# Kernel tuning notes

Measured on AMD Instinct MI355X. Metric: run time of the kernel, lower is better.

The kernel has to match this reference:

```python
import jax, jax.numpy as jnp
import numpy as np

B, S, D, H = 2, 2048, 1024, 16
HD = D // H  # 64


def setup_inputs() -> dict:
    key = jax.random.key(0)
    ks = jax.random.split(key, 6)
    x = jax.random.normal(ks[0], (B, S, D), dtype=jnp.float32)
    # rotary frequencies: theta = 10000^{-2i/hd}, angles = pos * theta
    inv_freq = 1.0 / (10000.0 ** (jnp.arange(0, HD, 2, dtype=jnp.float32) / HD))  # [HD/2]
    angles = jnp.arange(S, dtype=jnp.float32)[:, None] * inv_freq[None, :]  # [S, HD/2]
    freqs_cos = jnp.cos(angles)
    freqs_sin = jnp.sin(angles)
    scale = 0.02
    w_qkv = jax.random.normal(ks[1], (3 * D, D), dtype=jnp.float32) * scale
    b_qkv = jnp.zeros((3 * D,), dtype=jnp.float32)
    w_dense = jax.random.normal(ks[2], (D, D), dtype=jnp.float32) * scale
    b_dense = jnp.zeros((D,), dtype=jnp.float32)
    return {"x": x, "w_qkv": w_qkv, "b_qkv": b_qkv, "w_dense": w_dense,
            "b_dense": b_dense, "freqs_cos": freqs_cos, "freqs_sin": freqs_sin}


def _apply_rope(t, cos, sin):
    # t: [B, S, H, HD]; cos/sin: [S, HD/2] broadcast as [1, S, 1, HD/2]
    tr = t.reshape(t.shape[:-1] + (HD // 2, 2))
    x0, x1 = tr[..., 0], tr[..., 1]
    c = cos[None, :, None, :]
    s = sin[None, :, None, :]
    o0 = x0 * c - x1 * s  # real part of complex multiply
    o1 = x0 * s + x1 * c  # imag part
    return jnp.stack([o0, o1], axis=-1).reshape(t.shape)


def reference(x, w_qkv, b_qkv, w_dense, b_dense, freqs_cos, freqs_sin):
    b, s, d = x.shape
    qkv = x @ w_qkv.T + b_qkv              # [B, S, 3D]
    qkv = qkv.reshape(b, s, 3, H, HD)
    q, k, v = qkv[:, :, 0], qkv[:, :, 1], qkv[:, :, 2]  # [B, S, H, HD]
    q = _apply_rope(q, freqs_cos, freqs_sin)
    k = _apply_rope(k, freqs_cos, freqs_sin)
    # causal SDPA, scale = 1/sqrt(head_dim)
    q = q.transpose(0, 2, 1, 3)  # [B, H, S, HD]
    k = k.transpose(0, 2, 1, 3)
    v = v.transpose(0, 2, 1, 3)
    scores = jnp.einsum('bhqd,bhkd->bhqk', q, k) / jnp.sqrt(jnp.float32(HD))
    causal = jnp.tril(jnp.ones((s, s), dtype=bool))
    scores = jnp.where(causal[None, None], scores, jnp.finfo(scores.dtype).min)
    attn = jax.nn.softmax(scores, axis=-1)
    ctx = jnp.einsum('bhqk,bhkd->bhqd', attn, v)   # [B, H, S, HD]
    ctx = ctx.transpose(0, 2, 1, 3).reshape(b, s, d)
    return ctx @ w_dense.T + b_dense
```

## Files before the change

kernel.cpp:

```cpp
#include <hip/hip_runtime.h>
#include <stdint.h>

#define Bb 2
#define Ss 2048
#define Dd 1024
#define Hh 16
#define HDd 64

typedef float f32x4 __attribute__((ext_vector_type(4)));
typedef __bf16 bf16x8 __attribute__((ext_vector_type(8)));
typedef __bf16 bf16x2 __attribute__((ext_vector_type(2)));
typedef short s16x8 __attribute__((ext_vector_type(8)));

__device__ inline unsigned short f2bf(float f) {
  unsigned u = __builtin_bit_cast(unsigned, f);
  u += 0x7fffu + ((u >> 16) & 1u);
  return (unsigned short)(u >> 16);
}
__device__ inline float bf2f(unsigned short h) {
  unsigned u = ((unsigned)h) << 16;
  return __builtin_bit_cast(float, u);
}
__device__ inline unsigned pkcvt(float a, float b) {
  bf16x2 v;
  v[0] = (__bf16)a;
  v[1] = (__bf16)b;
  return __builtin_bit_cast(unsigned, v);
}
__device__ inline float ex2(float x) {
#if __has_builtin(__builtin_amdgcn_exp2f)
  return __builtin_amdgcn_exp2f(x);
#else
  float r;
  asm("v_exp_f32 %0, %1\n\ts_nop 1" : "=v"(r) : "v"(x));
  return r;
#endif
}
__device__ inline int swz(int row, int soff) {
  return (row << 6) + ((((soff >> 3) ^ (row & 7)) << 3) | (soff & 7));
}

#define GLDS(dst, src)                                                        \
  __builtin_amdgcn_global_load_lds(                                           \
      (const __attribute__((address_space(1))) void*)(src),                   \
      (__attribute__((address_space(3))) void*)(dst), 16, 0, 0)

__global__ void cast_all(const float* __restrict__ x, const float* __restrict__ wq,
                         const float* __restrict__ wd, unsigned short* __restrict__ dst) {
  int i = blockIdx.x * blockDim.x + threadIdx.x;
  float4 v;
  if (i < 1048576) v = ((const float4*)x)[i];
  else if (i < 1835008) v = ((const float4*)wq)[i - 1048576];
  else v = ((const float4*)wd)[i - 1835008];
  ushort4 o;
  o.x = f2bf(v.x); o.y = f2bf(v.y); o.z = f2bf(v.z); o.w = f2bf(v.w);
  ((ushort4*)dst)[i] = o;
}

__global__ __launch_bounds__(512, 2) void gemm_qkv(
    const unsigned short* __restrict__ A, const unsigned short* __restrict__ Bw,
    const float* __restrict__ bias, unsigned short* __restrict__ qkvout,
    unsigned short* __restrict__ vtout,
    const float* __restrict__ fc, const float* __restrict__ fs) {
  const int K = 1024, NT = 16;
  __shared__ __align__(16) unsigned short Ah[2][2][128 * 32];
  __shared__ __align__(16) unsigned short Bh[2][2][192 * 32];
  const int tid = threadIdx.x;
  const int w = tid >> 6, l = tid & 63;
  const int lg = l >> 4, lr = l & 15;
  const int wm = w >> 2, wn = w & 3;
  int id = blockIdx.y * gridDim.x + blockIdx.x;
  const int nwg = gridDim.x * gridDim.y;
  id = (id & 7) * (nwg >> 3) + (id >> 3);
  const int bx = id % gridDim.x, by = id / gridDim.x;
  const int mbase = by * 128, nbase = bx * 192;

  const unsigned short *as0, *bs0, *bs1, *bs2;
  {
    int r_ = tid >> 2, s_ = (tid & 3) ^ ((r_ >> 1) & 3);
    as0 = A + (size_t)(mbase + r_) * K + s_ * 8;
    bs0 = Bw + (size_t)(nbase + r_) * K + s_ * 8;
    int cb2 = 512 + tid;
    int h2 = cb2 >= 768;
    int cw2 = cb2 - h2 * 768;
    int r2 = cw2 >> 2, s2 = (cw2 & 3) ^ ((r2 >> 1) & 3);
    bs1 = Bw + (size_t)(nbase + r2) * K + h2 * 32 + s2 * 8;
    int cw3 = 256 + tid;
    int r3 = cw3 >> 2, s3 = (cw3 & 3) ^ ((r3 >> 1) & 3);
    bs2 = Bw + (size_t)(nbase + r3) * K + 32 + s3 * 8;
  }
#define STAGE(buf, k0)                                                        \
  GLDS(&Ah[buf][0][0] + tid * 8, as0 + (k0));                                 \
  GLDS(&Ah[buf][0][0] + 4096 + tid * 8, as0 + 32 + (k0));                     \
  GLDS(&Bh[buf][0][0] + tid * 8, bs0 + (k0));                                 \
  GLDS(&Bh[buf][0][0] + (512 + tid) * 8, bs1 + (k0));                         \
  GLDS(&Bh[buf][0][0] + (1024 + tid) * 8, bs2 + (k0));

  STAGE(0, 0);
  __syncthreads();

  f32x4 acc[4][3] = {};
  for (int t = 0; t < NT; ++t) {
    const int cur = t & 1;
    if (t + 1 < NT) { STAGE(cur ^ 1, (t + 1) * 64); }
#pragma unroll
    for (int h = 0; h < 2; ++h) {
      bf16x8 bfr[3], af[4];
#pragma unroll
      for (int ni = 0; ni < 3; ++ni) {
        int row = wn * 48 + ni * 16 + lr;
        bfr[ni] = *(const bf16x8*)(&Bh[cur][h][row * 32 + ((lg ^ ((row >> 1) & 3)) << 3)]);
      }
#pragma unroll
      for (int j = 0; j < 4; ++j) {
        int row = wm * 64 + j * 16 + lr;
        af[j] = *(const bf16x8*)(&Ah[cur][h][row * 32 + ((lg ^ ((row >> 1) & 3)) << 3)]);
      }
      __builtin_amdgcn_s_setprio(1);
#pragma unroll
      for (int j = 0; j < 4; ++j)
#pragma unroll
        for (int ni = 0; ni < 3; ++ni)
          acc[j][ni] = __builtin_amdgcn_mfma_f32_16x16x32_bf16(
              af[j], bfr[ni], acc[j][ni], 0, 0, 0);
      __builtin_amdgcn_s_setprio(0);
    }
    __syncthreads();
  }
#undef STAGE

#pragma unroll
  for (int mi = 0; mi < 4; ++mi)
#pragma unroll
    for (int ni = 0; ni < 3; ++ni) {
      int col = nbase + wn * 48 + ni * 16 + lr;
      float bi = bias[col];
      int row0 = mbase + wm * 64 + mi * 16 + lg * 4;
      float o4[4];
#pragma unroll
      for (int r = 0; r < 4; ++r) o4[r] = acc[mi][ni][r] + bi;
      int sect = col >> 10;
      int d = col & 63;
      int srow0 = row0 & 2047;
      if (sect < 2) {
        int p = d >> 1;
#pragma unroll
        for (int r = 0; r < 4; ++r) {
          float vp = __shfl_xor(o4[r], 1);
          float c = fc[(srow0 + r) * 32 + p];
          float s = fs[(srow0 + r) * 32 + p];
          float o = (d & 1) ? (vp * s + o4[r] * c) : (o4[r] * c - vp * s);
          qkvout[(size_t)(row0 + r) * 3072 + col] = f2bf(o);
        }
      } else {
        int bh = (row0 >> 11) * 16 + ((col >> 6) & 15);
        uint2 o;
        o.x = pkcvt(o4[0], o4[1]);
        o.y = pkcvt(o4[2], o4[3]);
        *(uint2*)&vtout[((size_t)(bh * 64 + d)) * 2048 + srow0] = o;
      }
    }
}

__global__ __launch_bounds__(256) void gemm_bt(
    const unsigned short* __restrict__ A, const unsigned short* __restrict__ Bw,
    const float* __restrict__ bias, float* __restrict__ Cout,
    int M, int N, int K) {
  __shared__ __align__(16) unsigned short As[128 * 32];
  __shared__ __align__(16) unsigned short Bs[128 * 32];
  const int tid = threadIdx.x;
  const int w = tid >> 6, l = tid & 63;
  const int lg = l >> 4, lr = l & 15;
  const int mbase = blockIdx.y * 128, nbase = blockIdx.x * 128;
  const int wr = w >> 1, wc = w & 1;
  f32x4 acc[4][4] = {};

  for (int k0 = 0; k0 < K; k0 += 32) {
#pragma unroll
    for (int r = 0; r < 2; ++r) {
      int c = r * 256 + w * 64 + l;
      int row = c >> 2, c8 = c & 3;
      GLDS(As + c * 8, A + (size_t)(mbase + row) * K + k0 + c8 * 8);
      GLDS(Bs + c * 8, Bw + (size_t)(nbase + row) * K + k0 + c8 * 8);
    }
    __syncthreads();
    bf16x8 af[4], bfr[4];
#pragma unroll
    for (int mi = 0; mi < 4; ++mi)
      af[mi] = *(const bf16x8*)(As + (wr * 64 + mi * 16 + lr) * 32 + lg * 8);
#pragma unroll
    for (int ni = 0; ni < 4; ++ni)
      bfr[ni] = *(const bf16x8*)(Bs + (wc * 64 + ni * 16 + lr) * 32 + lg * 8);
#pragma unroll
    for (int mi = 0; mi < 4; ++mi)
#pragma unroll
      for (int ni = 0; ni < 4; ++ni)
        acc[mi][ni] = __builtin_amdgcn_mfma_f32_16x16x32_bf16(
            af[mi], bfr[ni], acc[mi][ni], 0, 0, 0);
    __syncthreads();
  }

#pragma unroll
  for (int mi = 0; mi < 4; ++mi) {
#pragma unroll
    for (int ni = 0; ni < 4; ++ni) {
      int col = nbase + wc * 64 + ni * 16 + lr;
      float bi = bias[col];
#pragma unroll
      for (int r = 0; r < 4; ++r) {
        int row = mbase + wr * 64 + mi * 16 + lg * 4 + r;
        Cout[(size_t)row * N + col] = acc[mi][ni][r] + bi;
      }
    }
  }
}

__global__ __launch_bounds__(256, 3) void attn(
    const unsigned short* __restrict__ qkv, const unsigned short* __restrict__ vt,
    unsigned short* __restrict__ ctx) {
  __shared__ __align__(16) unsigned short Ks[2][64 * 64];
  __shared__ __align__(16) unsigned short Vs[2][64 * 64];
  __shared__ __align__(16) unsigned short Ps[4][32 * 64];
  int did = blockIdx.x;
  int x = did & 7, rest = did >> 3;
  int bh = x * 4 + (rest & 3);
  int qi = 31 - (rest >> 2);
  int b = bh >> 4, h = bh & 15;
  int qbase = qi * 64;
  int tid = threadIdx.x;
  int w = tid >> 6, l = tid & 63;
  int lg = l >> 4, lr = l & 15;
  int wq = w & 1, wk = w >> 1;
  int qw = wq * 32;

  bf16x8 qb[2][2];
#pragma unroll
  for (int mi = 0; mi < 2; ++mi)
#pragma unroll
    for (int kc = 0; kc < 2; ++kc) {
      s16x8 qr = *(const s16x8*)(qkv +
          (size_t)(b * Ss + qbase + qw + mi * 16 + lr) * 3072 + h * 64 + kc * 32 + lg * 8);
      bf16x8 qs;
#pragma unroll
      for (int e = 0; e < 8; ++e)
        qs[e] = (__bf16)(bf2f((unsigned short)qr[e]) * 0.18033688f);
      qb[mi][kc] = qs;
    }

  int c1 = tid, c2 = 256 + tid;
  int r1 = c1 >> 3, s1 = ((c1 & 7) ^ (r1 & 7)) * 8;
  int r2 = c2 >> 3, s2 = ((c2 & 7) ^ (r2 & 7)) * 8;
  const unsigned short* kg1 = qkv + ((size_t)(b * Ss) + r1) * 3072 + 1024 + h * 64 + s1;
  const unsigned short* kg2 = qkv + ((size_t)(b * Ss) + r2) * 3072 + 1024 + h * 64 + s2;
  const unsigned short* vg1 = vt + ((size_t)bh * 64 + r1) * 2048 + s1;
  const unsigned short* vg2 = vt + ((size_t)bh * 64 + r2) * 2048 + s2;
#define STAGEKV(kt)                                                           \
  {                                                                           \
    int tt_ = (kt) & 1;                                                       \
    GLDS(&Ks[tt_][0] + c1 * 8, kg1 + (size_t)(kt) * 64 * 3072);               \
    GLDS(&Ks[tt_][0] + c2 * 8, kg2 + (size_t)(kt) * 64 * 3072);               \
    GLDS(&Vs[tt_][0] + c1 * 8, vg1 + (kt) * 64);                              \
    GLDS(&Vs[tt_][0] + c2 * 8, vg2 + (kt) * 64);                              \
  }

  int nkt = qi + 1;
  int nsup = (nkt + 1) >> 1;

  STAGEKV(0);
  if (1 < nkt) STAGEKV(1);
  __syncthreads();

  f32x4 acc[4][2] = {};
  float mrow[2] = {-1e30f, -1e30f}, lsum[2] = {0.f, 0.f};

  for (int j = 0; j < nsup; ++j) {
    int kt = 2 * j + wk;
    if (kt < nkt) {
      f32x4 st[4][2] = {};
      __builtin_amdgcn_s_setprio(1);
#pragma unroll
      for (int kc = 0; kc < 2; ++kc) {
#pragma unroll
        for (int ni = 0; ni < 4; ++ni) {
          bf16x8 ka = *(const bf16x8*)&Ks[wk][swz(ni * 16 + lr, kc * 32 + lg * 8)];
#pragma unroll
          for (int mi = 0; mi < 2; ++mi)
            st[ni][mi] = __builtin_amdgcn_mfma_f32_16x16x32_bf16(
                ka, qb[mi][kc], st[ni][mi], 0, 0, 0);
        }
      }
      __builtin_amdgcn_s_setprio(0);

      float tm[2] = {-1e30f, -1e30f};
      if (kt == qi) {
#pragma unroll
        for (int mi = 0; mi < 2; ++mi) {
          int rq = qw + mi * 16 + lr;
#pragma unroll
          for (int ni = 0; ni < 4; ++ni)
#pragma unroll
            for (int r4 = 0; r4 < 4; ++r4) {
              float s = st[ni][mi][r4];
              if (ni * 16 + lg * 4 + r4 > rq) s = -1e30f;
              st[ni][mi][r4] = s;
              tm[mi] = fmaxf(tm[mi], s);
            }
        }
      } else {
#pragma unroll
        for (int mi = 0; mi < 2; ++mi)
#pragma unroll
          for (int ni = 0; ni < 4; ++ni)
#pragma unroll
            for (int r4 = 0; r4 < 4; ++r4) tm[mi] = fmaxf(tm[mi], st[ni][mi][r4]);
      }
      bool ok = (tm[0] <= mrow[0] + 8.0f) && (tm[1] <= mrow[1] + 8.0f);
      if (!__all(ok)) {
#pragma unroll
        for (int mi = 0; mi < 2; ++mi) {
          float t = fmaxf(tm[mi], __shfl_xor(tm[mi], 16));
          t = fmaxf(t, __shfl_xor(t, 32));
          float mnew = fmaxf(mrow[mi], t);
          float alpha = ex2(mrow[mi] - mnew);
          lsum[mi] *= alpha;
#pragma unroll
          for (int nd = 0; nd < 4; ++nd)
#pragma unroll
            for (int r4 = 0; r4 < 4; ++r4) acc[nd][mi][r4] *= alpha;
          mrow[mi] = mnew;
        }
      }
#pragma unroll
      for (int mi = 0; mi < 2; ++mi) {
        float sum = 0.f;
#pragma unroll
        for (int ni = 0; ni < 4; ++ni)
#pragma unroll
          for (int r4 = 0; r4 < 4; ++r4) {
            float pe = ex2(st[ni][mi][r4] - mrow[mi]);
            st[ni][mi][r4] = pe;
            sum += pe;
          }
        lsum[mi] += sum;
#pragma unroll
        for (int ni = 0; ni < 4; ++ni) {
          uint2 wv;
          wv.x = pkcvt(st[ni][mi][0], st[ni][mi][1]);
          wv.y = pkcvt(st[ni][mi][2], st[ni][mi][3]);
          *(uint2*)&Ps[w][swz(mi * 16 + lr, ni * 16 + lg * 4)] = wv;
        }
      }
      __builtin_amdgcn_s_setprio(1);
#pragma unroll
      for (int kc = 0; kc < 2; ++kc) {
        bf16x8 pbf[2];
#pragma unroll
        for (int mi = 0; mi < 2; ++mi)
          pbf[mi] = *(const bf16x8*)&Ps[w][swz(mi * 16 + lr, kc * 32 + lg * 8)];
#pragma unroll
        for (int nd = 0; nd < 4; ++nd) {
          bf16x8 va = *(const bf16x8*)&Vs[wk][swz(nd * 16 + lr, kc * 32 + lg * 8)];
#pragma unroll
          for (int mi = 0; mi < 2; ++mi)
            acc[nd][mi] = __builtin_amdgcn_mfma_f32_16x16x32_bf16(
                va, pbf[mi], acc[nd][mi], 0, 0, 0);
        }
      }
      __builtin_amdgcn_s_setprio(0);
    }

    if (j + 1 < nsup) {
      __syncthreads();
      int t0 = 2 * (j + 1), t1 = t0 + 1;
      STAGEKV(t0);
      if (t1 < nkt) STAGEKV(t1);
      __syncthreads();
    }
  }
#undef STAGEKV

#pragma unroll
  for (int mi = 0; mi < 2; ++mi) {
    lsum[mi] += __shfl_xor(lsum[mi], 16);
    lsum[mi] += __shfl_xor(lsum[mi], 32);
  }
  __syncthreads();
  float* aS0 = (float*)Ks;
  float* aS1 = (float*)Vs;
  float* mlS = (float*)Ps;
  if (wk == 1) {
    int base = (wq * 64 + l) * 16;
#pragma unroll
    for (int nd = 0; nd < 4; ++nd) {
      *(f32x4*)(aS0 + base + nd * 4) = acc[nd][0];
      *(f32x4*)(aS1 + base + nd * 4) = acc[nd][1];
    }
    int mb = (wq * 64 + l) * 4;
    mlS[mb] = mrow[0]; mlS[mb + 1] = lsum[0];
    mlS[mb + 2] = mrow[1]; mlS[mb + 3] = lsum[1];
  }
  __syncthreads();
  if (wk == 0) {
    int base = (wq * 64 + l) * 16;
    int mb = (wq * 64 + l) * 4;
#pragma unroll
    for (int mi = 0; mi < 2; ++mi) {
      const float* as = (mi ? aS1 : aS0) + base;
      float m1 = mlS[mb + mi * 2], l1 = mlS[mb + mi * 2 + 1];
      float M = fmaxf(mrow[mi], m1);
      float s0 = ex2(mrow[mi] - M), s1 = ex2(m1 - M);
      float inv = 1.0f / (lsum[mi] * s0 + l1 * s1);
      float f0 = s0 * inv, f1 = s1 * inv;
      int qg = qbase + qw + mi * 16 + lr;
#pragma unroll
      for (int nd = 0; nd < 4; ++nd) {
        f32x4 a1 = *(const f32x4*)(as + nd * 4);
        uint2 o;
        o.x = pkcvt(acc[nd][mi][0] * f0 + a1[0] * f1,
                    acc[nd][mi][1] * f0 + a1[1] * f1);
        o.y = pkcvt(acc[nd][mi][2] * f0 + a1[2] * f1,
                    acc[nd][mi][3] * f0 + a1[3] * f1);
        *(uint2*)&ctx[((size_t)(b * Ss) + qg) * 1024 + h * 64 + nd * 16 + lg * 4] = o;
      }
    }
  }
}

extern "C" void kernel_launch(void* const* d_in, const int* in_sizes, int n_in,
                              void* d_out, int out_size, void* d_ws, size_t ws_size,
                              hipStream_t stream) {
  const float* x       = (const float*)d_in[0];
  const float* w_qkv   = (const float*)d_in[1];
  const float* b_qkv   = (const float*)d_in[2];
  const float* w_dense = (const float*)d_in[3];
  const float* b_dense = (const float*)d_in[4];
  const float* fc      = (const float*)d_in[5];
  const float* fs      = (const float*)d_in[6];
  float* out = (float*)d_out;

  char* ws = (char*)d_ws;
  unsigned short* xb    = (unsigned short*)(ws);
  unsigned short* wqkvb = (unsigned short*)(ws + (8ull  << 20));
  unsigned short* wdb   = (unsigned short*)(ws + (14ull << 20));
  unsigned short* qkvb  = (unsigned short*)(ws + (16ull << 20));
  unsigned short* vt    = (unsigned short*)(ws + (40ull << 20));

  cast_all<<<8192, 256, 0, stream>>>(x, w_qkv, w_dense, xb);

  gemm_qkv<<<dim3(16, 32), 512, 0, stream>>>(xb, wqkvb, b_qkv, qkvb, vt, fc, fs);
  attn<<<1024, 256, 0, stream>>>(qkvb, vt, xb );
  gemm_bt<<<dim3(8, 32), 256, 0, stream>>>(xb, wdb, b_dense, out,
                                           4096, 1024, 1024);
}
```

Before: 104.5 us.

## Retile output GEMM to 64x128 blocks with swizzled LDS and XCD remap

The output projection GEMM now uses 64x128 tiles, giving 512 workgroups instead of 256, so more of the GPU's compute units have work. Shared-memory rows are XOR-swizzled to cut bank conflicts on the fragment reads. Block IDs are remapped across the 8 XCDs to improve cache locality, and MFMA sections are wrapped in s_setprio. Each block does less reuse per loaded tile, and the kernel still runs a single-buffered k-loop.

```diff
diff --git a/kernel.cpp b/kernel.cpp
--- a/kernel.cpp
+++ b/kernel.cpp
@@ -162,53 +162,68 @@
     }
 }
 
-__global__ __launch_bounds__(256) void gemm_bt(
+__global__ __launch_bounds__(256, 2) void gemm_out(
     const unsigned short* __restrict__ A, const unsigned short* __restrict__ Bw,
-    const float* __restrict__ bias, float* __restrict__ Cout,
-    int M, int N, int K) {
-  __shared__ __align__(16) unsigned short As[128 * 32];
+    const float* __restrict__ bias, float* __restrict__ Cout) {
+  const int M = 4096, N = 1024, K = 1024;
+  __shared__ __align__(16) unsigned short As[64 * 32];
   __shared__ __align__(16) unsigned short Bs[128 * 32];
   const int tid = threadIdx.x;
   const int w = tid >> 6, l = tid & 63;
   const int lg = l >> 4, lr = l & 15;
-  const int mbase = blockIdx.y * 128, nbase = blockIdx.x * 128;
-  const int wr = w >> 1, wc = w & 1;
-  f32x4 acc[4][4] = {};
-
+  const int wm = w >> 1, wn = w & 1;
+  int id = blockIdx.y * gridDim.x + blockIdx.x;
+  const int nwg = gridDim.x * gridDim.y;
+  id = (id & 7) * (nwg >> 3) + (id >> 3);
+  const int bx = id % gridDim.x, by = id / gridDim.x;
+  const int mbase = by * 64, nbase = bx * 128;
+
+  const unsigned short *as0, *bs0, *bs1;
+  {
+    int r_ = tid >> 2, s_ = (tid & 3) ^ ((r_ >> 1) & 3);
+    as0 = A + (size_t)(mbase + r_) * K + s_ * 8;
+    bs0 = Bw + (size_t)(nbase + r_) * K + s_ * 8;
+    int r2 = 64 + r_, s2 = (tid & 3) ^ ((r2 >> 1) & 3);
+    bs1 = Bw + (size_t)(nbase + r2) * K + s2 * 8;
+  }
+
+  f32x4 acc[2][4] = {};
   for (int k0 = 0; k0 < K; k0 += 32) {
-#pragma unroll
-    for (int r = 0; r < 2; ++r) {
-      int c = r * 256 + w * 64 + l;
-      int row = c >> 2, c8 = c & 3;
-      GLDS(As + c * 8, A + (size_t)(mbase + row) * K + k0 + c8 * 8);
-      GLDS(Bs + c * 8, Bw + (size_t)(nbase + row) * K + k0 + c8 * 8);
-    }
+    GLDS(As + tid * 8, as0 + k0);
+    GLDS(Bs + tid * 8, bs0 + k0);
+    GLDS(Bs + (256 + tid) * 8, bs1 + k0);
     __syncthreads();
-    bf16x8 af[4], bfr[4];
-#pragma unroll
-    for (int mi = 0; mi < 4; ++mi)
-      af[mi] = *(const bf16x8*)(As + (wr * 64 + mi * 16 + lr) * 32 + lg * 8);
-#pragma unroll
-    for (int ni = 0; ni < 4; ++ni)
-      bfr[ni] = *(const bf16x8*)(Bs + (wc * 64 + ni * 16 + lr) * 32 + lg * 8);
-#pragma unroll
-    for (int mi = 0; mi < 4; ++mi)
+    bf16x8 af[2], bfr[4];
+#pragma unroll
+    for (int mi = 0; mi < 2; ++mi) {
+      int row = wm * 32 + mi * 16 + lr;
+      af[mi] = *(const bf16x8*)(As + row * 32 + ((lg ^ ((row >> 1) & 3)) << 3));
+    }
+#pragma unroll
+    for (int ni = 0; ni < 4; ++ni) {
+      int row = wn * 64 + ni * 16 + lr;
+      bfr[ni] = *(const bf16x8*)(Bs + row * 32 + ((lg ^ ((row >> 1) & 3)) << 3));
+    }
+    __builtin_amdgcn_s_setprio(1);
+#pragma unroll
+    for (int mi = 0; mi < 2; ++mi)
 #pragma unroll
       for (int ni = 0; ni < 4; ++ni)
         acc[mi][ni] = __builtin_amdgcn_mfma_f32_16x16x32_bf16(
             af[mi], bfr[ni], acc[mi][ni], 0, 0, 0);
+    __builtin_amdgcn_s_setprio(0);
     __syncthreads();
   }
 
 #pragma unroll
-  for (int mi = 0; mi < 4; ++mi) {
+  for (int mi = 0; mi < 2; ++mi) {
 #pragma unroll
     for (int ni = 0; ni < 4; ++ni) {
-      int col = nbase + wc * 64 + ni * 16 + lr;
+      int col = nbase + wn * 64 + ni * 16 + lr;
       float bi = bias[col];
 #pragma unroll
       for (int r = 0; r < 4; ++r) {
-        int row = mbase + wr * 64 + mi * 16 + lg * 4 + r;
+        int row = mbase + wm * 32 + mi * 16 + lg * 4 + r;
         Cout[(size_t)row * N + col] = acc[mi][ni][r] + bi;
       }
     }
@@ -449,6 +464,5 @@
 
   gemm_qkv<<<dim3(16, 32), 512, 0, stream>>>(xb, wqkvb, b_qkv, qkvb, vt, fc, fs);
   attn<<<1024, 256, 0, stream>>>(qkvb, vt, xb );
-  gemm_bt<<<dim3(8, 32), 256, 0, stream>>>(xb, wdb, b_dense, out,
-                                           4096, 1024, 1024);
-}
+  gemm_out<<<dim3(8, 64), 256, 0, stream>>>(xb, wdb, b_dense, out);
+}
```

After: 96.62 us (median of 3 runs). -7.6%, faster.
